# Kernel optimization log

Measured on AMD Instinct MI355X. Metric: run time of the kernel, lower is better.

The kernel has to match this reference:

```python
import jax, jax.numpy as jnp
from jax import lax
import numpy as np

B, N_WAY, K_SHOT, Q, IMG = 8, 5, 1, 15, 84
D = 3      # repnet spatial output for imgsz=84
CF = 64    # repnet channels
C2 = CF + 2

def _conv(x, w, b):
    y = lax.conv_general_dilated(x, w, (1, 1), 'VALID', dimension_numbers=('NCHW', 'OIHW', 'NCHW'))
    return y + b[None, :, None, None]

def _maxpool2(x):
    return lax.reduce_window(x, -jnp.inf, lax.max, (1, 1, 2, 2), (1, 1, 2, 2), 'VALID')

def _avgpool5(x):
    return lax.reduce_window(x, 0.0, lax.add, (1, 1, 5, 5), (1, 1, 5, 5), 'VALID') / 25.0

def _bn(x, g, b):
    # train-mode BatchNorm2d: batch statistics over (N, H, W), biased variance, eps=1e-5
    m = jnp.mean(x, (0, 2, 3), keepdims=True)
    v = jnp.var(x, (0, 2, 3), keepdims=True)
    return (x - m) * lax.rsqrt(v + 1e-5) * g[None, :, None, None] + b[None, :, None, None]

def _repnet(x, cw1, cb1, bg1, bb1, cw2, cb2, bg2, bb2, cw3, cb3, bg3, bb3, cw4, cb4, bg4, bb4):
    x = jax.nn.relu(_bn(_maxpool2(_conv(x, cw1, cb1)), bg1, bb1))
    x = jax.nn.relu(_bn(_maxpool2(_conv(x, cw2, cb2)), bg2, bb2))
    x = jax.nn.relu(_bn(_conv(x, cw3, cb3), bg3, bb3))
    x = jax.nn.relu(_bn(_conv(x, cw4, cb4), bg4, bb4))
    return _avgpool5(x)

def _forward(support_x, support_y, query_x, query_y, cw1, cb1, bg1, bb1, cw2, cb2, bg2, bb2, cw3, cb3, bg3, bb3, cw4, cb4, bg4, bb4, gW1, gb1, gW2, gb2, gW3, gb3, gW4, gb4, fW1, fb1, fW2, fb2, fW3, fb3, fW4, fb4):
    b, setsz = support_x.shape[:2]
    q = query_x.shape[1]
    rep = lambda z: _repnet(z, cw1, cb1, bg1, bb1, cw2, cb2, bg2, bb2, cw3, cb3, bg3, bb3, cw4, cb4, bg4, bb4)
    sup = rep(support_x.reshape(b * setsz, 3, IMG, IMG)).reshape(b, setsz, CF, D, D)
    qry = rep(query_x.reshape(b * q, 3, IMG, IMG)).reshape(b, q, CF, D, D)
    sup = sup.reshape(b, N_WAY, K_SHOT, CF, D, D).sum(2)  # sum over shots -> (b, n_way, c, d, d)
    setsz = N_WAY
    sy = support_y[:, ::K_SHOT]
    ii, jj = jnp.meshgrid(jnp.arange(D), jnp.arange(D), indexing='ij')
    coord = jnp.stack([ii, jj]).astype(jnp.float32) / D  # (2, d, d): ch0 = i/d, ch1 = j/d
    sup = jnp.concatenate([sup, jnp.broadcast_to(coord, (b, setsz, 2, D, D))], axis=2)  # (b,s,66,d,d)
    qry = jnp.concatenate([qry, jnp.broadcast_to(coord, (b, q, 2, D, D))], axis=2)      # (b,q,66,d,d)
    d2 = D * D
    sup = sup.reshape(b, setsz, C2, d2)
    qry = qry.reshape(b, q, C2, d2)
    # pair feature is cat([support_feat, query_feat]); split g's first layer so the
    # (b,q,s,d2,d2,2c) pair tensor is never materialized: g1([s;q]) = s@Ws + q@Wq + b1
    Ws, Wq = gW1[:C2], gW1[C2:]
    A = jnp.einsum('bscp,ck->bspk', sup, Ws)   # (b, s, d2, 256)
    Bq = jnp.einsum('bqcp,ck->bqpk', qry, Wq)  # (b, q, d2, 256)
    h = jax.nn.relu(A[:, None, :, :, None, :] + Bq[:, :, None, None, :, :] + gb1)  # (b,q,s,d2,d2,256)
    h = jax.nn.relu(h @ gW2 + gb2)
    h = jax.nn.relu(h @ gW3 + gb3)
    h = jax.nn.relu(h @ gW4 + gb4)
    x_f = h.sum((3, 4))  # sum over all d2*d2 pixel pairs -> (b, q, s, 256)
    h = jax.nn.relu(x_f @ fW1 + fb1)
    h = jax.nn.relu(h @ fW2 + fb2)  # nn.Dropout treated as identity (deterministic reference)
    h = jax.nn.relu(h @ fW3 + fb3)
    o = h @ fW4 + fb4  # (b, q, s, 64)
    score = jnp.sqrt(jnp.sum(o * o, axis=-1))  # L2 norm over feature dim -> (b, q, s)
    n = jnp.sqrt(jnp.sum(score * score, axis=2, keepdims=True))
    score = score / n * (n * n / (1.0 + n * n))  # squash
    ap = sy[:, None, :] == query_y[:, :, None]  # exactly one True per (b, q)
    an = ~ap
    score_ap = jnp.sum(jnp.where(ap, score, 0.0), axis=2, keepdims=True)
    MARGIN = 0.2
    loss = jnp.sum(jax.nn.relu(score - score_ap + MARGIN) * an)
    return loss

def setup_inputs() -> dict:
    key = jax.random.key(0)
    ks = iter(jax.random.split(key, 48))
    nrm = lambda shape, s: jax.random.normal(next(ks), shape, jnp.float32) * s
    inp = {}
    inp['support_x'] = nrm((B, N_WAY * K_SHOT, 3, IMG, IMG), 1.0)
    inp['support_y'] = jnp.tile(jnp.arange(N_WAY, dtype=jnp.int32), (B, 1))
    inp['query_x'] = nrm((B, Q, 3, IMG, IMG), 1.0)
    inp['query_y'] = jax.random.randint(next(ks), (B, Q), 0, N_WAY, dtype=jnp.int32)
    inp['cw1'] = nrm((64, 3, 3, 3), 0.19); inp['cb1'] = nrm((64,), 0.02)
    inp['bg1'] = 1.0 + nrm((64,), 0.05); inp['bb1'] = nrm((64,), 0.02)
    inp['cw2'] = nrm((64, 64, 3, 3), 0.042); inp['cb2'] = nrm((64,), 0.02)
    inp['bg2'] = 1.0 + nrm((64,), 0.05); inp['bb2'] = nrm((64,), 0.02)
    inp['cw3'] = nrm((64, 64, 3, 3), 0.042); inp['cb3'] = nrm((64,), 0.02)
    inp['bg3'] = 1.0 + nrm((64,), 0.05); inp['bb3'] = nrm((64,), 0.02)
    inp['cw4'] = nrm((64, 64, 3, 3), 0.042); inp['cb4'] = nrm((64,), 0.02)
    inp['bg4'] = 1.0 + nrm((64,), 0.05); inp['bb4'] = nrm((64,), 0.02)
    inp['gW1'] = nrm((2 * C2, 256), 0.087); inp['gb1'] = nrm((256,), 0.02)
    inp['gW2'] = nrm((256, 256), 0.0625); inp['gb2'] = nrm((256,), 0.02)
    inp['gW3'] = nrm((256, 256), 0.0625); inp['gb3'] = nrm((256,), 0.02)
    inp['gW4'] = nrm((256, 256), 0.0625); inp['gb4'] = nrm((256,), 0.02)
    inp['fW1'] = nrm((256, 256), 0.0625); inp['fb1'] = nrm((256,), 0.02)
    inp['fW2'] = nrm((256, 256), 0.0625); inp['fb2'] = nrm((256,), 0.02)
    inp['fW3'] = nrm((256, 128), 0.0625); inp['fb3'] = nrm((128,), 0.02)
    inp['fW4'] = nrm((128, 64), 0.088); inp['fb4'] = nrm((64,), 0.02)
    return inp

def reference(support_x, support_y, query_x, query_y, cw1, cb1, bg1, bb1, cw2, cb2, bg2, bb2, cw3, cb3, bg3, bb3, cw4, cb4, bg4, bb4, gW1, gb1, gW2, gb2, gW3, gb3, gW4, gb4, fW1, fb1, fW2, fb2, fW3, fb3, fW4, fb4):
    return _forward(support_x, support_y, query_x, query_y, cw1, cb1, bg1, bb1, cw2, cb2, bg2, bb2, cw3, cb3, bg3, bb3, cw4, cb4, bg4, bb4, gW1, gb1, gW2, gb2, gW3, gb3, gW4, gb4, fW1, fb1, fW2, fb2, fW3, fb3, fW4, fb4)
```

## Files before the change

### kernel.cpp

```cpp
#include <hip/hip_runtime.h>
#include <hip/hip_bf16.h>

typedef __hip_bfloat16 bf16;
typedef __attribute__((ext_vector_type(8))) short short8;
typedef __attribute__((ext_vector_type(4))) short bfx4;
typedef __attribute__((ext_vector_type(4))) float f32x4;

#define DEV __device__ __forceinline__

static constexpr int NSUP = 40;
static constexpr int NQRY = 120;
static constexpr int NIMG = 160;
static constexpr int GM   = 48600;
static constexpr int GMP  = 48640;
static constexpr int NBS  = 128;
static constexpr int NBQ  = 384;

DEV float b2f(short s) {
    union { unsigned int u; float f; } v; v.u = ((unsigned int)(unsigned short)s) << 16; return v.f;
}
DEV short bfbits(float v) {
    bf16 h = __float2bfloat16(v);
    union { bf16 b; short s; } u; u.b = h; return u.s;
}

DEV int xcd_swz(int b, int nwg) {
    int q = nwg >> 3, r = nwg & 7;
    int x = b & 7, i = b >> 3;
    return (x < r) ? x * (q + 1) + i : r * (q + 1) + (x - r) * q + i;
}

#define GLL(gp, lp) __builtin_amdgcn_global_load_lds( \
    (const __attribute__((address_space(1))) void*)(gp), \
    (__attribute__((address_space(3))) void*)(lp), 16, 0, 0)

__global__ void nhwc4_kernel(const float* sx, const float* qx, bf16* img) {
    int idx = blockIdx.x * 256 + threadIdx.x;
    if (idx >= NIMG * 7056) return;
    int n = idx / 7056, p = idx % 7056;
    const float* im = ((n < NSUP) ? sx + (size_t)n * 3 * 7056 : qx + (size_t)(n - NSUP) * 3 * 7056) + p;
    bfx4 o;
    o[0] = bfbits(im[0]);
    o[1] = bfbits(im[7056]);
    o[2] = bfbits(im[14112]);
    o[3] = 0;
    *(bfx4*)&img[(size_t)idx * 4] = o;
}

__global__ void prep_kernel(const float* cw1, const float* cw2, const float* cw3,
                            const float* cw4, const float* gW2, const float* gW3,
                            const float* gW4, const float* fW1, const float* fW2,
                            const float* fW3, const float* fW4, const float* fb4,
                            bf16* Wc1, bf16* Wp, bf16* WTg, bf16* fWT, float* fb4p) {
    int idx = blockIdx.x * 256 + threadIdx.x;
    if (idx < 4096) {
        int oc = idx >> 6, k = idx & 63;
        int ky = k >> 4, r = k & 15;
        float v = 0.f;
        if (ky < 3 && r < 12) {
            int kx = r >> 2, ic = r & 3;
            if (ic < 3) v = cw1[oc * 27 + ic * 9 + ky * 3 + kx];
        }
        Wc1[idx] = __float2bfloat16(v);
        return;
    }
    idx -= 4096;
    if (idx < 3 * 64 * 584) {
        int L = idx / (64 * 584), r = idx % (64 * 584);
        int oc = r / 584, kk = r % 584;
        const float* src = (L == 0) ? cw2 : (L == 1) ? cw3 : cw4;
        float v = 0.f;
        if (kk < 576) {
            int ic = kk & 63, tap = kk >> 6;
            v = src[oc * 576 + ic * 9 + tap];
        }
        Wp[idx] = __float2bfloat16(v);
        return;
    }
    idx -= 3 * 64 * 584;
    if (idx < 3 * 65536) {
        int L = idx >> 16, r = idx & 65535, n = r >> 8, k = r & 255;
        const float* W = (L == 0) ? gW2 : (L == 1) ? gW3 : gW4;
        WTg[idx] = __float2bfloat16(W[k * 256 + n]);
        return;
    }
    idx -= 3 * 65536;
    if (idx < 65536) {
        int n = idx >> 8, k = idx & 255;
        fWT[idx] = __float2bfloat16(fW1[k * 256 + n]);
    } else if (idx < 131072) {
        int r = idx - 65536, n = r >> 8, k = r & 255;
        fWT[idx] = __float2bfloat16(fW2[k * 256 + n]);
    } else if (idx < 163840) {
        int r = idx - 131072, n = r >> 8, k = r & 255;
        fWT[idx] = __float2bfloat16(fW3[k * 128 + n]);
    } else if (idx < 180224) {
        int r = idx - 163840, n = r >> 7, k = r & 127;
        float v = (n < 64) ? fW4[k * 64 + n] : 0.f;
        fWT[idx] = __float2bfloat16(v);
    } else if (idx < 180352) {
        int i = idx - 180224;
        fb4p[i] = (i < 64) ? fb4[i] : 0.f;
    }
}

__global__ __launch_bounds__(256) void conv1m_kernel(
        const bf16* __restrict__ img, const bf16* __restrict__ Wc1,
        const float* __restrict__ cb1, bf16* __restrict__ out) {
    int wid = xcd_swz(blockIdx.x, NIMG * 27);
    int n = wid / 27, chunk = wid % 27;
    int wv = threadIdx.x >> 6, ln = threadIdx.x & 63;
    int pr = ln & 15, kg = ln >> 4;
    int t0 = (chunk * 4 + wv) * 16;
    int t = t0 + pr;
    int tc = t < 1681 ? t : 1680;
    int pyt = tc / 41, pxt = tc % 41;
    const bf16* ib = img + (size_t)n * 28224;

    short8 wf[4][2];
    #pragma unroll
    for (int mt = 0; mt < 4; ++mt)
        #pragma unroll
        for (int h = 0; h < 2; ++h)
            wf[mt][h] = *(const short8*)&Wc1[(size_t)(mt * 16 + pr) * 64 + h * 32 + kg * 8];

    int r8 = (kg & 1) * 8;
    int kyb = kg >> 1;
    short8 pf[4][2];
    #pragma unroll
    for (int nt = 0; nt < 4; ++nt) {
        int py = 2 * pyt + (nt >> 1), px = 2 * pxt + (nt & 1);
        #pragma unroll
        for (int h = 0; h < 2; ++h) {
            int ky = h * 2 + kyb;
            short8 f = {0, 0, 0, 0, 0, 0, 0, 0};
            if (ky < 3) {
                const bf16* p = ib + ((py + ky) * 84 + px) * 4 + r8;
                if (r8 == 0) {
                    bfx4 a0 = *(const bfx4*)p, a1 = *(const bfx4*)(p + 4);
                    f[0] = a0[0]; f[1] = a0[1]; f[2] = a0[2]; f[3] = a0[3];
                    f[4] = a1[0]; f[5] = a1[1]; f[6] = a1[2]; f[7] = a1[3];
                } else {
                    bfx4 a0 = *(const bfx4*)p;
                    f[0] = a0[0]; f[1] = a0[1]; f[2] = a0[2]; f[3] = a0[3];
                }
            }
            pf[nt][h] = f;
        }
    }

    f32x4 acc[4][4];
    #pragma unroll
    for (int a = 0; a < 4; ++a)
        #pragma unroll
        for (int b = 0; b < 4; ++b)
            #pragma unroll
            for (int r = 0; r < 4; ++r) acc[a][b][r] = 0.f;

    #pragma unroll
    for (int h = 0; h < 2; ++h)
        #pragma unroll
        for (int mt = 0; mt < 4; ++mt)
            #pragma unroll
            for (int nt = 0; nt < 4; ++nt)
                acc[mt][nt] = __builtin_amdgcn_mfma_f32_16x16x32_bf16(
                    wf[mt][h], pf[nt][h], acc[mt][nt], 0, 0, 0);

    if (t < 1681) {
        bf16* ob = out + ((size_t)n * 1681 + t) * 64;
        #pragma unroll
        for (int mt = 0; mt < 4; ++mt) {
            f32x4 v = acc[mt][0];
            #pragma unroll
            for (int nt = 1; nt < 4; ++nt)
                #pragma unroll
                for (int r = 0; r < 4; ++r) v[r] = fmaxf(v[r], acc[mt][nt][r]);
            bfx4 o;
            #pragma unroll
            for (int r = 0; r < 4; ++r) o[r] = bfbits(v[r] + cb1[mt * 16 + kg * 4 + r]);
            *(bfx4*)&ob[mt * 16 + kg * 4] = o;
        }
    }
}

__global__ void stats_nhwc_kernel(const bf16* buf, int HW, float* partial) {
    int blk = blockIdx.x;
    bool qg = blk >= NBS;
    int b0 = qg ? blk - NBS : blk;
    int nb = qg ? NBQ : NBS;
    const bf16* base = buf + (qg ? (size_t)NSUP * HW * 64 : 0);
    long rows = (long)(qg ? NQRY : NSUP) * HW;
    int tid = threadIdx.x;
    int sub = tid & 7, rl = tid >> 3;
    float s1[8], s2[8];
    #pragma unroll
    for (int j = 0; j < 8; ++j) { s1[j] = 0.f; s2[j] = 0.f; }
    for (long r = (long)b0 * 32 + rl; r < rows; r += (long)nb * 32) {
        short8 v = *(const short8*)&base[r * 64 + sub * 8];
        #pragma unroll
        for (int j = 0; j < 8; ++j) { float f = b2f(v[j]); s1[j] += f; s2[j] += f * f; }
    }
    __shared__ float l1[256][8], l2[256][8];
    #pragma unroll
    for (int j = 0; j < 8; ++j) { l1[tid][j] = s1[j]; l2[tid][j] = s2[j]; }
    __syncthreads();
    if (tid < 64) {
        int su = tid >> 3, j = tid & 7;
        float a = 0.f, b = 0.f;
        for (int k = 0; k < 32; ++k) { a += l1[su + k * 8][j]; b += l2[su + k * 8][j]; }
        partial[blk * 128 + tid] = a;
        partial[blk * 128 + 64 + tid] = b;
    }
}

__global__ __launch_bounds__(1024) void bnfin_kernel(
        const float* partial, const float* gam, const float* bet,
        int HW, float* scsh) {
    int tid = threadIdx.x;
    int out = tid >> 3;
    int part = tid & 7;
    int g = out >> 6, c = out & 63;
    int b0 = g ? NBS : 0, nb = g ? NBQ : NBS;
    float s1 = 0.f, s2 = 0.f;
    for (int b = b0 + part; b < b0 + nb; b += 8) {
        s1 += partial[b * 128 + c];
        s2 += partial[b * 128 + 64 + c];
    }
    __shared__ float r1[1024], r2[1024];
    r1[tid] = s1; r2[tid] = s2;
    __syncthreads();
    if (part == 0) {
        #pragma unroll
        for (int j = 1; j < 8; ++j) { s1 += r1[tid + j]; s2 += r2[tid + j]; }
        float cnt = (float)((g ? NQRY : NSUP)) * (float)HW;
        float mean = s1 / cnt;
        float var = s2 / cnt - mean * mean;
        float istd = rsqrtf(var + 1e-5f);
        float sc = gam[c] * istd;
        scsh[out] = sc;
        scsh[128 + out] = bet[c] - mean * sc;
    }
}

__global__ void bnrelu_nhwc_kernel(bf16* buf, const float* scsh, int HW, int total8) {
    int idx = blockIdx.x * 256 + threadIdx.x;
    if (idx >= total8) return;
    size_t e0 = (size_t)idx * 8;
    int c0 = (int)(e0 & 63);
    int g = (int)(e0 / ((size_t)HW * 64)) >= NSUP ? 1 : 0;
    short8 v = *(short8*)&buf[e0];
    short8 o;
    #pragma unroll
    for (int j = 0; j < 8; ++j) {
        int c = c0 + j;
        float f = b2f(v[j]) * scsh[g * 64 + c] + scsh[128 + g * 64 + c];
        o[j] = bfbits(fmaxf(f, 0.f));
    }
    *(short8*)&buf[e0] = o;
}

template <int IW, int OW, bool POOL, int NT>
__global__ __launch_bounds__(256) void convmfma_kernel(
        const bf16* __restrict__ in, const bf16* __restrict__ Wp,
        const float* __restrict__ cb, bf16* __restrict__ out, int nwg) {
    constexpr int M  = OW * OW;
    constexpr int PW = OW / 2;
    constexpr int MP = POOL ? PW * PW : M;
    constexpr int T  = NIMG * MP;
    constexpr int NPF = POOL ? 4 : NT;

    int wid = xcd_swz(blockIdx.x, nwg);
    int wv = threadIdx.x >> 6, ln = threadIdx.x & 63;
    int pr = ln & 15, kg = ln >> 4;

    const bf16* pptr[NPF];
    int pxv[NPF];
    if (POOL) {
        int gp = (wid * 4 + wv) * 16 + pr;
        int gpc = gp < T ? gp : T - 1;
        pxv[0] = gp;
        int n = gpc / MP, pp = gpc % MP;
        int py = pp / PW, px = pp % PW;
        const bf16* ib = in + (size_t)n * (IW * IW * 64) + kg * 8;
        #pragma unroll
        for (int nt = 0; nt < 4; ++nt)
            pptr[nt] = ib + ((2 * py + (nt >> 1)) * IW + 2 * px + (nt & 1)) * 64;
    } else {
        #pragma unroll
        for (int nt = 0; nt < NT; ++nt) {
            int gp = (wid * 4 + wv) * (16 * NT) + nt * 16 + pr;
            int gpc = gp < T ? gp : T - 1;
            pxv[nt] = gp;
            int n = gpc / M, pix = gpc % M;
            int y = pix / OW, x = pix % OW;
            pptr[nt] = in + ((size_t)n * (IW * IW) + y * IW + x) * 64 + kg * 8;
        }
    }
    const bf16* wb = Wp + kg * 8;

    f32x4 acc[4][NPF];
    #pragma unroll
    for (int a = 0; a < 4; ++a)
        #pragma unroll
        for (int b = 0; b < NPF; ++b)
            #pragma unroll
            for (int r = 0; r < 4; ++r) acc[a][b][r] = 0.f;

    short8 pf_c[NPF];
    #pragma unroll
    for (int nt = 0; nt < NPF; ++nt) pf_c[nt] = *(const short8*)(pptr[nt]);
    #pragma unroll
    for (int s = 0; s < 18; ++s) {
        short8 pf_n[NPF];
        if (s < 17) {
            int s2 = s + 1, tap2 = s2 >> 1, h2 = s2 & 1;
            int off2 = ((tap2 / 3) * IW + (tap2 % 3)) * 64 + h2 * 32;
            #pragma unroll
            for (int nt = 0; nt < NPF; ++nt)
                pf_n[nt] = *(const short8*)(pptr[nt] + off2);
        }
        int wk = s * 32;
        short8 wf[4];
        #pragma unroll
        for (int mt = 0; mt < 4; ++mt)
            wf[mt] = *(const short8*)(wb + (size_t)(mt * 16 + pr) * 584 + wk);
        #pragma unroll
        for (int mt = 0; mt < 4; ++mt)
            #pragma unroll
            for (int nt = 0; nt < NPF; ++nt)
                acc[mt][nt] = __builtin_amdgcn_mfma_f32_16x16x32_bf16(
                    wf[mt], pf_c[nt], acc[mt][nt], 0, 0, 0);
        if (s < 17) {
            #pragma unroll
            for (int nt = 0; nt < NPF; ++nt) pf_c[nt] = pf_n[nt];
        }
    }

    if (POOL) {
        int gp = pxv[0];
        if (gp < T) {
            bf16* ob = out + (size_t)gp * 64;
            #pragma unroll
            for (int mt = 0; mt < 4; ++mt) {
                f32x4 v = acc[mt][0];
                #pragma unroll
                for (int nt = 1; nt < 4; ++nt)
                    #pragma unroll
                    for (int r = 0; r < 4; ++r) v[r] = fmaxf(v[r], acc[mt][nt][r]);
                bfx4 o;
                #pragma unroll
                for (int r = 0; r < 4; ++r) o[r] = bfbits(v[r] + cb[mt * 16 + kg * 4 + r]);
                *(bfx4*)&ob[mt * 16 + kg * 4] = o;
            }
        }
    } else {
        #pragma unroll
        for (int mt = 0; mt < 4; ++mt) {
            float bv[4];
            #pragma unroll
            for (int r = 0; r < 4; ++r) bv[r] = cb[mt * 16 + kg * 4 + r];
            #pragma unroll
            for (int nt = 0; nt < NPF; ++nt) {
                if (pxv[nt] < T) {
                    bfx4 o;
                    #pragma unroll
                    for (int r = 0; r < 4; ++r) o[r] = bfbits(acc[mt][nt][r] + bv[r]);
                    *(bfx4*)&out[(size_t)pxv[nt] * 64 + mt * 16 + kg * 4] = o;
                }
            }
        }
    }
}

__global__ void bnpool_kernel(const bf16* buf4, const float* scsh, float* feat) {
    int wid = blockIdx.x * 4 + (threadIdx.x >> 6);
    int c = threadIdx.x & 63;
    if (wid >= 1440) return;
    int n = wid / 9, p9 = wid % 9;
    int g = n >= NSUP;
    float sc = scsh[g * 64 + c], sh = scsh[128 + g * 64 + c];
    int ii = p9 / 3, jj = p9 % 3;
    const bf16* base = buf4 + ((size_t)n * 225 + ii * 5 * 15 + jj * 5) * 64 + c;
    float s = 0;
    #pragma unroll
    for (int u = 0; u < 5; ++u)
        #pragma unroll
        for (int v = 0; v < 5; ++v)
            s += fmaxf(__bfloat162float(base[(u * 15 + v) * 64]) * sc + sh, 0.f);
    feat[n * 576 + c * 9 + p9] = s * 0.04f;
}

__global__ void proj_kernel(const float* feat, const float* gW1, float* A, float* Bq) {
    int n = blockIdx.x, k = threadIdx.x;
    const float* W = (n < NSUP) ? gW1 : gW1 + 66 * 256;
    float* out = (n < NSUP) ? A + (size_t)n * 9 * 256 : Bq + (size_t)(n - NSUP) * 9 * 256;
    const float* fb = feat + n * 576;
    for (int p = 0; p < 9; ++p) {
        float acc = 0;
        for (int c = 0; c < 64; ++c) acc += fb[c * 9 + p] * W[c * 256 + k];
        acc += ((float)(p / 3) * (1.f / 3.f)) * W[64 * 256 + k];
        acc += ((float)(p % 3) * (1.f / 3.f)) * W[65 * 256 + k];
        out[p * 256 + k] = acc;
    }
}

__global__ void h0_kernel(const float* A, const float* Bq, const float* gb1, bf16* H) {
    int tid = threadIdx.x;
    int row = blockIdx.x * 8 + (tid >> 5);
    int col = (tid & 31) * 8;
    short8 o;
    if (row < GM) {
        int bqs = row / 81, r81 = row % 81;
        int ps = r81 / 9, pq = r81 % 9;
        int b = bqs / 75, r75 = bqs % 75, q = r75 / 5, s = r75 % 5;
        const float* Ar = A + ((size_t)((b * 5 + s) * 9 + ps)) * 256 + col;
        const float* Br = Bq + ((size_t)((b * 15 + q) * 9 + pq)) * 256 + col;
        #pragma unroll
        for (int j = 0; j < 8; ++j) {
            float v = Ar[j] + Br[j] + gb1[col + j];
            o[j] = bfbits(fmaxf(v, 0.f));
        }
    } else {
        #pragma unroll
        for (int j = 0; j < 8; ++j) o[j] = 0;
    }
    *(short8*)&H[(size_t)row * 256 + col] = o;
}

template <int KT, bool RELU, bool F32OUT>
__global__ __launch_bounds__(256) void gemm_f_kernel(
        const bf16* __restrict__ Ain, const bf16* __restrict__ WT,
        const float* __restrict__ bias, void* __restrict__ outv, int ldo) {
    constexpr int K = KT * 32;
    __shared__ __align__(16) short As[2][4096];
    __shared__ __align__(16) short Bs[2][4096];
    int bm0 = blockIdx.x * 128;
    int bn0 = blockIdx.y * 128;
    int tid = threadIdx.x, wv = tid >> 6, ln = tid & 63;
    int wm = wv >> 1, wn = wv & 1;

    int srow = (wv * 2) * 16 + (ln >> 2);
    int scol = (ln & 3) * 8;
    const bf16* Ag = Ain + (size_t)(bm0 + srow) * K + scol;
    const bf16* Bg = WT + (size_t)(bn0 + srow) * K + scol;

    f32x4 acc[4][4];
    #pragma unroll
    for (int m = 0; m < 4; ++m)
        #pragma unroll
        for (int n = 0; n < 4; ++n)
            #pragma unroll
            for (int r = 0; r < 4; ++r) acc[m][n][r] = 0.f;

    int ar = (wm * 64 + (ln & 15)) * 32 + (ln >> 4) * 8;
    int br = (wn * 64 + (ln & 15)) * 32 + (ln >> 4) * 8;

    GLL(Ag,          &As[0][(wv * 2) * 512]);
    GLL(Ag + 16 * K, &As[0][(wv * 2 + 1) * 512]);
    GLL(Bg,          &Bs[0][(wv * 2) * 512]);
    GLL(Bg + 16 * K, &Bs[0][(wv * 2 + 1) * 512]);
    __syncthreads();

    int cur = 0;
    for (int kt = 0; kt < KT; ++kt) {
        if (kt < KT - 1) {
            int k0 = (kt + 1) * 32;
            GLL(Ag + k0,          &As[cur ^ 1][(wv * 2) * 512]);
            GLL(Ag + 16 * K + k0, &As[cur ^ 1][(wv * 2 + 1) * 512]);
            GLL(Bg + k0,          &Bs[cur ^ 1][(wv * 2) * 512]);
            GLL(Bg + 16 * K + k0, &Bs[cur ^ 1][(wv * 2 + 1) * 512]);
        }
        short8 a[4], b[4];
        #pragma unroll
        for (int m = 0; m < 4; ++m) a[m] = *(const short8*)&As[cur][ar + m * 512];
        #pragma unroll
        for (int n = 0; n < 4; ++n) b[n] = *(const short8*)&Bs[cur][br + n * 512];
        #pragma unroll
        for (int m = 0; m < 4; ++m)
            #pragma unroll
            for (int n = 0; n < 4; ++n)
                acc[m][n] = __builtin_amdgcn_mfma_f32_16x16x32_bf16(a[m], b[n], acc[m][n], 0, 0, 0);
        __syncthreads();
        cur ^= 1;
    }

    int orow = bm0 + wm * 64 + (ln >> 4) * 4;
    int ocol = bn0 + wn * 64 + (ln & 15);
    #pragma unroll
    for (int n = 0; n < 4; ++n) {
        float bv = bias[ocol + n * 16];
        #pragma unroll
        for (int m = 0; m < 4; ++m) {
            #pragma unroll
            for (int r = 0; r < 4; ++r) {
                float v = acc[m][n][r] + bv;
                if (RELU) v = fmaxf(v, 0.f);
                size_t oi = (size_t)(orow + m * 16 + r) * ldo + ocol + n * 16;
                if (F32OUT) ((float*)outv)[oi] = v;
                else        ((bf16*)outv)[oi] = __float2bfloat16(v);
            }
        }
    }
}

__global__ void xfred_kernel(const bf16* H, bf16* xfb) {
    int bqs = blockIdx.x, tid = threadIdx.x;
    int sub = tid & 31, rl = tid >> 5;
    float s[8];
    #pragma unroll
    for (int j = 0; j < 8; ++j) s[j] = 0.f;
    if (bqs < 600) {
        const bf16* p = H + (size_t)bqs * 81 * 256 + sub * 8;
        for (int r = rl; r < 81; r += 8) {
            short8 v = *(const short8*)&p[r * 256];
            #pragma unroll
            for (int j = 0; j < 8; ++j) s[j] += b2f(v[j]);
        }
    }
    __shared__ float red[256][8];
    #pragma unroll
    for (int j = 0; j < 8; ++j) red[tid][j] = s[j];
    __syncthreads();
    if (tid < 32) {
        short8 o;
        #pragma unroll
        for (int j = 0; j < 8; ++j) {
            float t = 0;
            #pragma unroll
            for (int k = 0; k < 8; ++k) t += red[k * 32 + tid][j];
            o[j] = bfbits(t);
        }
        *(short8*)&xfb[(size_t)bqs * 256 + tid * 8] = o;
    }
}

__global__ void score_kernel(const float* F4, const int* sy, const int* qy, float* lossp) {
    __shared__ float scs[8];
    int bid = blockIdx.x;
    int tid = threadIdx.x;
    int s = tid >> 6, k = tid & 63;
    float v = F4[(size_t)(bid * 5 + s) * 128 + k];
    float sum = v * v;
    #pragma unroll
    for (int m = 1; m < 64; m <<= 1) sum += __shfl_xor(sum, m);
    if (k == 0) scs[s] = sqrtf(sum);
    __syncthreads();
    if (tid == 0) {
        int b = bid / 15, q = bid % 15;
        float n2 = 0;
        for (int j = 0; j < 5; ++j) n2 += scs[j] * scs[j];
        float n = sqrtf(n2);
        float f = n / (1.f + n2);
        int qyv = qy[b * 15 + q];
        float sc[5]; bool ap[5]; float sap = 0;
        for (int j = 0; j < 5; ++j) {
            sc[j] = scs[j] * f;
            ap[j] = (sy[b * 5 + j] == qyv);
            if (ap[j]) sap += sc[j];
        }
        float lp = 0;
        for (int j = 0; j < 5; ++j)
            if (!ap[j]) lp += fmaxf(sc[j] - sap + 0.2f, 0.f);
        lossp[bid] = lp;
    }
}

__global__ void lreduce_kernel(const float* lossp, float* out) {
    __shared__ float r[128];
    int tid = threadIdx.x;
    r[tid] = (tid < NQRY) ? lossp[tid] : 0.f;
    __syncthreads();
    for (int off = 64; off; off >>= 1) {
        if (tid < off) r[tid] += r[tid + off];
        __syncthreads();
    }
    if (tid == 0) out[0] = r[0];
}

extern "C" void kernel_launch(void* const* d_in, const int* in_sizes, int n_in,
                              void* d_out, int out_size, void* d_ws, size_t ws_size,
                              hipStream_t stream) {
    const float* sx  = (const float*)d_in[0];
    const int*   syp = (const int*)d_in[1];
    const float* qx  = (const float*)d_in[2];
    const int*   qyp = (const int*)d_in[3];
    const float* cw1 = (const float*)d_in[4];  const float* cb1 = (const float*)d_in[5];
    const float* bg1 = (const float*)d_in[6];  const float* bb1 = (const float*)d_in[7];
    const float* cw2 = (const float*)d_in[8];  const float* cb2 = (const float*)d_in[9];
    const float* bg2 = (const float*)d_in[10]; const float* bb2 = (const float*)d_in[11];
    const float* cw3 = (const float*)d_in[12]; const float* cb3 = (const float*)d_in[13];
    const float* bg3 = (const float*)d_in[14]; const float* bb3 = (const float*)d_in[15];
    const float* cw4 = (const float*)d_in[16]; const float* cb4 = (const float*)d_in[17];
    const float* bg4 = (const float*)d_in[18]; const float* bb4 = (const float*)d_in[19];
    const float* gW1 = (const float*)d_in[20]; const float* gb1 = (const float*)d_in[21];
    const float* gW2 = (const float*)d_in[22]; const float* gb2 = (const float*)d_in[23];
    const float* gW3 = (const float*)d_in[24]; const float* gb3 = (const float*)d_in[25];
    const float* gW4 = (const float*)d_in[26]; const float* gb4 = (const float*)d_in[27];
    const float* fW1 = (const float*)d_in[28]; const float* fb1 = (const float*)d_in[29];
    const float* fW2 = (const float*)d_in[30]; const float* fb2 = (const float*)d_in[31];
    const float* fW3 = (const float*)d_in[32]; const float* fb3 = (const float*)d_in[33];
    const float* fW4 = (const float*)d_in[34]; const float* fb4 = (const float*)d_in[35];

    char* w = (char*)d_ws;
    size_t off = 0;
    bf16*  buf1  = (bf16*)(w + off); off += 34426880ull;
    bf16*  hbuf  = (bf16*)(w + off); off += 31150080ull;
    bf16*  pbuf2 = (bf16*)(w + off); off += 7393280ull;
    bf16*  buf3  = (bf16*)(w + off); off += 5918720ull;
    bf16*  buf4  = (bf16*)(w + off); off += 4608000ull;
    float* feat  = (float*)(w + off); off += 368640ull;
    float* Abuf  = (float*)(w + off); off += 368640ull;
    float* Bbuf  = (float*)(w + off); off += 1105920ull;
    bf16*  xfb   = (bf16*)(w + off); off += 327680ull;
    bf16*  F1    = (bf16*)(w + off); off += 327680ull;
    bf16*  F2    = (bf16*)(w + off); off += 327680ull;
    bf16*  F3    = (bf16*)(w + off); off += 163840ull;
    float* F4    = (float*)(w + off); off += 327680ull;
    float* partial = (float*)(w + off); off += 262144ull;
    float* scsh  = (float*)(w + off); off += 4096ull;
    bf16*  imgN  = (bf16*)(w + off); off += 9031680ull;
    bf16*  Wc1   = (bf16*)(w + off); off += 8192ull;
    bf16*  Wp    = (bf16*)(w + off); off += 224256ull;
    bf16*  WTg   = (bf16*)(w + off); off += 393216ull;
    bf16*  fWT   = (bf16*)(w + off); off += 360448ull;
    float* fb4p  = (float*)(w + off); off += 512ull;
    float* lossp = (float*)(w + off); off += 512ull;

    float* scsh1 = scsh;        float* scsh2 = scsh + 256;
    float* scsh3 = scsh + 512;  float* scsh4 = scsh + 768;
    bf16* Wp2 = Wp;
    bf16* Wp3 = Wp + 64 * 584;
    bf16* Wp4 = Wp + 2 * 64 * 584;
    bf16* fWT1 = fWT;
    bf16* fWT2 = fWT + 65536;
    bf16* fWT3 = fWT + 131072;
    bf16* fWT4 = fWT + 163840;

    bf16* Hb0 = buf1;
    bf16* Hb1 = hbuf;

    nhwc4_kernel<<<(NIMG * 7056 + 255) / 256, 256, 0, stream>>>(sx, qx, imgN);
    prep_kernel<<<(493184 + 255) / 256, 256, 0, stream>>>(
        cw1, cw2, cw3, cw4, gW2, gW3, gW4, fW1, fW2, fW3, fW4, fb4,
        Wc1, Wp, WTg, fWT, fb4p);

    conv1m_kernel<<<NIMG * 27, 256, 0, stream>>>(imgN, Wc1, cb1, buf1);
    stats_nhwc_kernel<<<NBS + NBQ, 256, 0, stream>>>(buf1, 1681, partial);
    bnfin_kernel<<<1, 1024, 0, stream>>>(partial, bg1, bb1, 1681, scsh1);
    bnrelu_nhwc_kernel<<<(2151680 + 255) / 256, 256, 0, stream>>>(buf1, scsh1, 1681, 2151680);

    convmfma_kernel<41, 39, true, 4><<<dim3(903), 256, 0, stream>>>(buf1, Wp2, cb2, pbuf2, 903);
    stats_nhwc_kernel<<<NBS + NBQ, 256, 0, stream>>>(pbuf2, 361, partial);
    bnfin_kernel<<<1, 1024, 0, stream>>>(partial, bg2, bb2, 361, scsh2);
    bnrelu_nhwc_kernel<<<(462080 + 255) / 256, 256, 0, stream>>>(pbuf2, scsh2, 361, 462080);

    convmfma_kernel<19, 17, false, 2><<<dim3(362), 256, 0, stream>>>(pbuf2, Wp3, cb3, buf3, 362);
    stats_nhwc_kernel<<<NBS + NBQ, 256, 0, stream>>>(buf3, 289, partial);
    bnfin_kernel<<<1, 1024, 0, stream>>>(partial, bg3, bb3, 289, scsh3);
    bnrelu_nhwc_kernel<<<(369920 + 255) / 256, 256, 0, stream>>>(buf3, scsh3, 289, 369920);

    convmfma_kernel<17, 15, false, 2><<<dim3(282), 256, 0, stream>>>(buf3, Wp4, cb4, buf4, 282);
    stats_nhwc_kernel<<<NBS + NBQ, 256, 0, stream>>>(buf4, 225, partial);
    bnfin_kernel<<<1, 1024, 0, stream>>>(partial, bg4, bb4, 225, scsh4);
    bnpool_kernel<<<360, 256, 0, stream>>>(buf4, scsh4, feat);

    proj_kernel<<<NIMG, 256, 0, stream>>>(feat, gW1, Abuf, Bbuf);

    h0_kernel<<<GMP / 8, 256, 0, stream>>>(Abuf, Bbuf, gb1, Hb0);
    dim3 ggrid(GMP / 128, 2);
    gemm_f_kernel<8, true, false><<<ggrid, 256, 0, stream>>>(Hb0, WTg,          gb2, (void*)Hb1, 256);
    gemm_f_kernel<8, true, false><<<ggrid, 256, 0, stream>>>(Hb1, WTg + 65536,  gb3, (void*)Hb0, 256);
    gemm_f_kernel<8, true, false><<<ggrid, 256, 0, stream>>>(Hb0, WTg + 131072, gb4, (void*)Hb1, 256);
    xfred_kernel<<<640, 256, 0, stream>>>(Hb1, xfb);

    gemm_f_kernel<8, true,  false><<<dim3(5, 2), 256, 0, stream>>>(xfb, fWT1, fb1,  (void*)F1, 256);
    gemm_f_kernel<8, true,  false><<<dim3(5, 2), 256, 0, stream>>>(F1,  fWT2, fb2,  (void*)F2, 256);
    gemm_f_kernel<8, true,  false><<<dim3(5, 1), 256, 0, stream>>>(F2,  fWT3, fb3,  (void*)F3, 128);
    gemm_f_kernel<4, false, true ><<<dim3(5, 1), 256, 0, stream>>>(F3,  fWT4, fb4p, (void*)F4, 128);

    score_kernel<<<NQRY, 320, 0, stream>>>(F4, syp, qyp, lossp);
    lreduce_kernel<<<1, 128, 0, stream>>>(lossp, (float*)d_out);
}
```

Before: 358.3 us.

## Fuse small kernels via last-block atomic reductions to cut launch count

Folds the image NHWC conversion into the prep kernel and resets the counters there. The BN-finalize kernels are merged into the stats kernels through a last-block-done atomic counter, and the final loss reduction is merged into the score kernel the same way. Avgpool and projection become one per-image kernel. This removes about ten tiny launches and their serialization gaps, in exchange for threadfence and atomic overhead and a single-block serial tail inside the stats kernels.

```diff
diff --git a/kernel.cpp b/kernel.cpp
--- a/kernel.cpp
+++ b/kernel.cpp
@@ -34,25 +34,28 @@
     (const __attribute__((address_space(1))) void*)(gp), \
     (__attribute__((address_space(3))) void*)(lp), 16, 0, 0)
 
-__global__ void nhwc4_kernel(const float* sx, const float* qx, bf16* img) {
-    int idx = blockIdx.x * 256 + threadIdx.x;
-    if (idx >= NIMG * 7056) return;
-    int n = idx / 7056, p = idx % 7056;
-    const float* im = ((n < NSUP) ? sx + (size_t)n * 3 * 7056 : qx + (size_t)(n - NSUP) * 3 * 7056) + p;
-    bfx4 o;
-    o[0] = bfbits(im[0]);
-    o[1] = bfbits(im[7056]);
-    o[2] = bfbits(im[14112]);
-    o[3] = 0;
-    *(bfx4*)&img[(size_t)idx * 4] = o;
-}
-
-__global__ void prep_kernel(const float* cw1, const float* cw2, const float* cw3,
+__global__ void prep_kernel(const float* sx, const float* qx, bf16* img,
+                            const float* cw1, const float* cw2, const float* cw3,
                             const float* cw4, const float* gW2, const float* gW3,
                             const float* gW4, const float* fW1, const float* fW2,
                             const float* fW3, const float* fW4, const float* fb4,
-                            bf16* Wc1, bf16* Wp, bf16* WTg, bf16* fWT, float* fb4p) {
-    int idx = blockIdx.x * 256 + threadIdx.x;
+                            bf16* Wc1, bf16* Wp, bf16* WTg, bf16* fWT, float* fb4p,
+                            int* counters) {
+    long gid = (long)blockIdx.x * 256 + threadIdx.x;
+    if (gid < 8) counters[gid] = 0;
+    if (gid < (long)NIMG * 7056) {
+        int n = (int)(gid / 7056), p = (int)(gid % 7056);
+        const float* im = ((n < NSUP) ? sx + (size_t)n * 3 * 7056
+                                      : qx + (size_t)(n - NSUP) * 3 * 7056) + p;
+        bfx4 o;
+        o[0] = bfbits(im[0]);
+        o[1] = bfbits(im[7056]);
+        o[2] = bfbits(im[14112]);
+        o[3] = 0;
+        *(bfx4*)&img[gid * 4] = o;
+        return;
+    }
+    int idx = (int)(gid - (long)NIMG * 7056);
     if (idx < 4096) {
         int oc = idx >> 6, k = idx & 63;
         int ky = k >> 4, r = k & 15;
@@ -183,7 +186,11 @@
     }
 }
 
-__global__ void stats_nhwc_kernel(const bf16* buf, int HW, float* partial) {
+__global__ void stats_nhwc_kernel(const bf16* buf, int HW, float* partial,
+                                  const float* gam, const float* bet,
+                                  float* scsh, int* counter) {
+    __shared__ float l1[256][8], l2[256][8];
+    __shared__ int isLast;
     int blk = blockIdx.x;
     bool qg = blk >= NBS;
     int b0 = qg ? blk - NBS : blk;
@@ -200,7 +207,6 @@
         #pragma unroll
         for (int j = 0; j < 8; ++j) { float f = b2f(v[j]); s1[j] += f; s2[j] += f * f; }
     }
-    __shared__ float l1[256][8], l2[256][8];
     #pragma unroll
     for (int j = 0; j < 8; ++j) { l1[tid][j] = s1[j]; l2[tid][j] = s2[j]; }
     __syncthreads();
@@ -211,30 +217,28 @@
         partial[blk * 128 + tid] = a;
         partial[blk * 128 + 64 + tid] = b;
     }
-}
-
-__global__ __launch_bounds__(1024) void bnfin_kernel(
-        const float* partial, const float* gam, const float* bet,
-        int HW, float* scsh) {
-    int tid = threadIdx.x;
-    int out = tid >> 3;
-    int part = tid & 7;
+    __threadfence();
+    __syncthreads();
+    if (tid == 0) isLast = (atomicAdd(counter, 1) == (NBS + NBQ) - 1);
+    __syncthreads();
+    if (!isLast) return;
+
+    int out = tid >> 1, part = tid & 1;
     int g = out >> 6, c = out & 63;
-    int b0 = g ? NBS : 0, nb = g ? NBQ : NBS;
-    float s1 = 0.f, s2 = 0.f;
-    for (int b = b0 + part; b < b0 + nb; b += 8) {
-        s1 += partial[b * 128 + c];
-        s2 += partial[b * 128 + 64 + c];
-    }
-    __shared__ float r1[1024], r2[1024];
-    r1[tid] = s1; r2[tid] = s2;
+    int fb0 = g ? NBS : 0, fnb = g ? NBQ : NBS;
+    float f1 = 0.f, f2 = 0.f;
+    for (int b = fb0 + part; b < fb0 + fnb; b += 2) {
+        f1 += partial[b * 128 + c];
+        f2 += partial[b * 128 + 64 + c];
+    }
+    l1[tid][0] = f1; l2[tid][0] = f2;
     __syncthreads();
     if (part == 0) {
-        #pragma unroll
-        for (int j = 1; j < 8; ++j) { s1 += r1[tid + j]; s2 += r2[tid + j]; }
+        f1 += l1[tid + 1][0];
+        f2 += l2[tid + 1][0];
         float cnt = (float)((g ? NQRY : NSUP)) * (float)HW;
-        float mean = s1 / cnt;
-        float var = s2 / cnt - mean * mean;
+        float mean = f1 / cnt;
+        float var = f2 / cnt - mean * mean;
         float istd = rsqrtf(var + 1e-5f);
         float sc = gam[c] * istd;
         scsh[out] = sc;
@@ -372,32 +376,32 @@
     }
 }
 
-__global__ void bnpool_kernel(const bf16* buf4, const float* scsh, float* feat) {
-    int wid = blockIdx.x * 4 + (threadIdx.x >> 6);
-    int c = threadIdx.x & 63;
-    if (wid >= 1440) return;
-    int n = wid / 9, p9 = wid % 9;
+__global__ void bnpool_proj_kernel(const bf16* buf4, const float* scsh,
+                                   const float* gW1, float* A, float* Bq) {
+    __shared__ float fs[576];
+    int n = blockIdx.x;
     int g = n >= NSUP;
-    float sc = scsh[g * 64 + c], sh = scsh[128 + g * 64 + c];
-    int ii = p9 / 3, jj = p9 % 3;
-    const bf16* base = buf4 + ((size_t)n * 225 + ii * 5 * 15 + jj * 5) * 64 + c;
-    float s = 0;
-    #pragma unroll
-    for (int u = 0; u < 5; ++u)
-        #pragma unroll
-        for (int v = 0; v < 5; ++v)
-            s += fmaxf(__bfloat162float(base[(u * 15 + v) * 64]) * sc + sh, 0.f);
-    feat[n * 576 + c * 9 + p9] = s * 0.04f;
-}
-
-__global__ void proj_kernel(const float* feat, const float* gW1, float* A, float* Bq) {
-    int n = blockIdx.x, k = threadIdx.x;
-    const float* W = (n < NSUP) ? gW1 : gW1 + 66 * 256;
-    float* out = (n < NSUP) ? A + (size_t)n * 9 * 256 : Bq + (size_t)(n - NSUP) * 9 * 256;
-    const float* fb = feat + n * 576;
+    int tid = threadIdx.x;
+    for (int e = tid; e < 576; e += 256) {
+        int c = e / 9, p9 = e % 9;
+        float sc = scsh[g * 64 + c], sh = scsh[128 + g * 64 + c];
+        int ii = p9 / 3, jj = p9 % 3;
+        const bf16* base = buf4 + ((size_t)n * 225 + ii * 5 * 15 + jj * 5) * 64 + c;
+        float s = 0;
+        #pragma unroll
+        for (int u = 0; u < 5; ++u)
+            #pragma unroll
+            for (int v = 0; v < 5; ++v)
+                s += fmaxf(__bfloat162float(base[(u * 15 + v) * 64]) * sc + sh, 0.f);
+        fs[e] = s * 0.04f;
+    }
+    __syncthreads();
+    int k = tid;
+    const float* W = g ? gW1 + 66 * 256 : gW1;
+    float* out = g ? Bq + (size_t)(n - NSUP) * 9 * 256 : A + (size_t)n * 9 * 256;
     for (int p = 0; p < 9; ++p) {
         float acc = 0;
-        for (int c = 0; c < 64; ++c) acc += fb[c * 9 + p] * W[c * 256 + k];
+        for (int c = 0; c < 64; ++c) acc += fs[c * 9 + p] * W[c * 256 + k];
         acc += ((float)(p / 3) * (1.f / 3.f)) * W[64 * 256 + k];
         acc += ((float)(p % 3) * (1.f / 3.f)) * W[65 * 256 + k];
         out[p * 256 + k] = acc;
@@ -534,8 +538,11 @@
     }
 }
 
-__global__ void score_kernel(const float* F4, const int* sy, const int* qy, float* lossp) {
+__global__ void score_kernel(const float* F4, const int* sy, const int* qy,
+                             float* lossp, float* outp, int* counter) {
     __shared__ float scs[8];
+    __shared__ int isLast;
+    __shared__ float r[128];
     int bid = blockIdx.x;
     int tid = threadIdx.x;
     int s = tid >> 6, k = tid & 63;
@@ -563,18 +570,18 @@
             if (!ap[j]) lp += fmaxf(sc[j] - sap + 0.2f, 0.f);
         lossp[bid] = lp;
     }
-}
-
-__global__ void lreduce_kernel(const float* lossp, float* out) {
-    __shared__ float r[128];
-    int tid = threadIdx.x;
-    r[tid] = (tid < NQRY) ? lossp[tid] : 0.f;
-    __syncthreads();
-    for (int off = 64; off; off >>= 1) {
-        if (tid < off) r[tid] += r[tid + off];
+    __threadfence();
+    __syncthreads();
+    if (tid == 0) isLast = (atomicAdd(counter, 1) == gridDim.x - 1);
+    __syncthreads();
+    if (!isLast) return;
+    if (tid < 128) r[tid] = (tid < NQRY) ? lossp[tid] : 0.f;
+    __syncthreads();
+    for (int off2 = 64; off2; off2 >>= 1) {
+        if (tid < off2) r[tid] += r[tid + off2];
         __syncthreads();
     }
-    if (tid == 0) out[0] = r[0];
+    if (tid == 0) outp[0] = r[0];
 }
 
 extern "C" void kernel_launch(void* const* d_in, const int* in_sizes, int n_in,
@@ -608,7 +615,6 @@
     bf16*  pbuf2 = (bf16*)(w + off); off += 7393280ull;
     bf16*  buf3  = (bf16*)(w + off); off += 5918720ull;
     bf16*  buf4  = (bf16*)(w + off); off += 4608000ull;
-    float* feat  = (float*)(w + off); off += 368640ull;
     float* Abuf  = (float*)(w + off); off += 368640ull;
     float* Bbuf  = (float*)(w + off); off += 1105920ull;
     bf16*  xfb   = (bf16*)(w + off); off += 327680ull;
@@ -625,6 +631,7 @@
     bf16*  fWT   = (bf16*)(w + off); off += 360448ull;
     float* fb4p  = (float*)(w + off); off += 512ull;
     float* lossp = (float*)(w + off); off += 512ull;
+    int*   counters = (int*)(w + off); off += 64ull;
 
     float* scsh1 = scsh;        float* scsh2 = scsh + 256;
     float* scsh3 = scsh + 512;  float* scsh4 = scsh + 768;
@@ -639,32 +646,25 @@
     bf16* Hb0 = buf1;
     bf16* Hb1 = hbuf;
 
-    nhwc4_kernel<<<(NIMG * 7056 + 255) / 256, 256, 0, stream>>>(sx, qx, imgN);
-    prep_kernel<<<(493184 + 255) / 256, 256, 0, stream>>>(
-        cw1, cw2, cw3, cw4, gW2, gW3, gW4, fW1, fW2, fW3, fW4, fb4,
-        Wc1, Wp, WTg, fWT, fb4p);
+    prep_kernel<<<(1128960 + 493184 + 255) / 256, 256, 0, stream>>>(
+        sx, qx, imgN, cw1, cw2, cw3, cw4, gW2, gW3, gW4,
+        fW1, fW2, fW3, fW4, fb4, Wc1, Wp, WTg, fWT, fb4p, counters);
 
     conv1m_kernel<<<NIMG * 27, 256, 0, stream>>>(imgN, Wc1, cb1, buf1);
-    stats_nhwc_kernel<<<NBS + NBQ, 256, 0, stream>>>(buf1, 1681, partial);
-    bnfin_kernel<<<1, 1024, 0, stream>>>(partial, bg1, bb1, 1681, scsh1);
+    stats_nhwc_kernel<<<NBS + NBQ, 256, 0, stream>>>(buf1, 1681, partial, bg1, bb1, scsh1, counters + 0);
     bnrelu_nhwc_kernel<<<(2151680 + 255) / 256, 256, 0, stream>>>(buf1, scsh1, 1681, 2151680);
 
     convmfma_kernel<41, 39, true, 4><<<dim3(903), 256, 0, stream>>>(buf1, Wp2, cb2, pbuf2, 903);
-    stats_nhwc_kernel<<<NBS + NBQ, 256, 0, stream>>>(pbuf2, 361, partial);
-    bnfin_kernel<<<1, 1024, 0, stream>>>(partial, bg2, bb2, 361, scsh2);
+    stats_nhwc_kernel<<<NBS + NBQ, 256, 0, stream>>>(pbuf2, 361, partial, bg2, bb2, scsh2, counters + 1);
     bnrelu_nhwc_kernel<<<(462080 + 255) / 256, 256, 0, stream>>>(pbuf2, scsh2, 361, 462080);
 
     convmfma_kernel<19, 17, false, 2><<<dim3(362), 256, 0, stream>>>(pbuf2, Wp3, cb3, buf3, 362);
-    stats_nhwc_kernel<<<NBS + NBQ, 256, 0, stream>>>(buf3, 289, partial);
-    bnfin_kernel<<<1, 1024, 0, stream>>>(partial, bg3, bb3, 289, scsh3);
+    stats_nhwc_kernel<<<NBS + NBQ, 256, 0, stream>>>(buf3, 289, partial, bg3, bb3, scsh3, counters + 2);
     bnrelu_nhwc_kernel<<<(369920 + 255) / 256, 256, 0, stream>>>(buf3, scsh3, 289, 369920);
 
     convmfma_kernel<17, 15, false, 2><<<dim3(282), 256, 0, stream>>>(buf3, Wp4, cb4, buf4, 282);
-    stats_nhwc_kernel<<<NBS + NBQ, 256, 0, stream>>>(buf4, 225, partial);
-    bnfin_kernel<<<1, 1024, 0, stream>>>(partial, bg4, bb4, 225, scsh4);
-    bnpool_kernel<<<360, 256, 0, stream>>>(buf4, scsh4, feat);
-
-    proj_kernel<<<NIMG, 256, 0, stream>>>(feat, gW1, Abuf, Bbuf);
+    stats_nhwc_kernel<<<NBS + NBQ, 256, 0, stream>>>(buf4, 225, partial, bg4, bb4, scsh4, counters + 3);
+    bnpool_proj_kernel<<<NIMG, 256, 0, stream>>>(buf4, scsh4, gW1, Abuf, Bbuf);
 
     h0_kernel<<<GMP / 8, 256, 0, stream>>>(Abuf, Bbuf, gb1, Hb0);
     dim3 ggrid(GMP / 128, 2);
@@ -678,6 +678,5 @@
     gemm_f_kernel<8, true,  false><<<dim3(5, 1), 256, 0, stream>>>(F2,  fWT3, fb3,  (void*)F3, 128);
     gemm_f_kernel<4, false, true ><<<dim3(5, 1), 256, 0, stream>>>(F3,  fWT4, fb4p, (void*)F4, 128);
 
-    score_kernel<<<NQRY, 320, 0, stream>>>(F4, syp, qyp, lossp);
-    lreduce_kernel<<<1, 128, 0, stream>>>(lossp, (float*)d_out);
-}
+    score_kernel<<<NQRY, 320, 0, stream>>>(F4, syp, qyp, lossp, (float*)d_out, counters + 4);
+}
```

Result: slower. 648.3 us (+81.0%).
